# Performance work log

Measured on AMD Instinct MI355X. Metric: run time of the kernel, lower is better.

## Reference

```python
import jax, jax.numpy as jnp
import numpy as np

N_NODES = 50000
N_GRAPHS = 128
IN_DIM = 512
HID = 512
N_LAYERS = 3


def setup_inputs() -> dict:
    key = jax.random.key(0)
    ks = jax.random.split(key, 12)
    inp = {
        "x": jax.random.normal(ks[0], (N_NODES, IN_DIM), dtype=jnp.float32),
        "walk2": jax.random.randint(ks[1], (3, N_NODES), 0, N_NODES, dtype=jnp.int32),
        "walk3": jax.random.randint(ks[2], (4, N_NODES), 0, N_NODES, dtype=jnp.int32),
        "walk4": jax.random.randint(ks[3], (5, N_NODES), 0, N_NODES, dtype=jnp.int32),
        "batch": jnp.sort(jax.random.randint(ks[4], (N_NODES,), 0, N_GRAPHS, dtype=jnp.int32)),
    }
    dims = [IN_DIM, HID, HID]
    for i in range(N_LAYERS):
        scale = 1.0 / np.sqrt(dims[i])
        inp[f"W{i}"] = jax.random.normal(ks[5 + i], (dims[i], HID), dtype=jnp.float32) * scale
        inp[f"b{i}"] = jnp.zeros((HID,), dtype=jnp.float32)
    return inp


def _gather_sum(z, walk):
    # walk: [L, N] node indices -> sum of gathered embeddings, [N, H]
    L, N = walk.shape
    return jnp.take(z, walk.reshape(-1), axis=0).reshape(L, N, z.shape[1]).sum(0)


def reference(x, walk2, walk3, walk4, batch, W0, b0, W1, b1, W2, b2):
    layers = [(W0, b0), (W1, b1), (W2, b2)]
    path_batch = jnp.take(batch, walk2[0])  # [N]
    counts = jax.ops.segment_sum(jnp.ones((path_batch.shape[0],), jnp.float32),
                                 path_batch, num_segments=N_GRAPHS)
    denom = jnp.maximum(counts, 1.0)[:, None]  # avoid div-by-zero for empty graphs
    z = x
    g = []
    for W, b in layers:
        z = z @ W + b  # [N, H]
        path_emb = _gather_sum(z, walk2) + _gather_sum(z, walk3) + _gather_sum(z, walk4)
        pooled = jax.ops.segment_sum(path_emb, path_batch, num_segments=N_GRAPHS) / denom
        g.append(pooled)
    return jnp.concatenate(g, axis=1)  # [N_GRAPHS, 3*H]
```

## Files before the change

kernel.cpp:

```cpp
#include <hip/hip_runtime.h>

#define N_NODES 50000
#define N_GRAPHS 128
#define HID 512

#define KSPAN  208
#define KSPLIT 241
#define KPAD   (KSPAN * KSPLIT)

#define C8_OFF     0
#define C8_BYTES   ((size_t)N_GRAPHS * KPAD)
#define PSUM_OFF   (C8_OFF + C8_BYTES)
#define PSUM_BYTES ((size_t)N_GRAPHS * HID * 4)
#define COUNTS_OFF (PSUM_OFF + PSUM_BYTES)
#define ZERO_BYTES (COUNTS_OFF + 512)
#define CBF_OFF    ZERO_BYTES
#define CBF_BYTES  (2 * C8_BYTES)
#define PART_OFF   (CBF_OFF + CBF_BYTES)
#define PART_BYTES ((size_t)KSPLIT * N_GRAPHS * HID * 4)

typedef __attribute__((ext_vector_type(8))) short bf16x8;
typedef __attribute__((ext_vector_type(16))) float f32x16;

__global__ __launch_bounds__(256)
void build_c_kernel(const int* __restrict__ w2, const int* __restrict__ w3,
                    const int* __restrict__ w4, const int* __restrict__ batch,
                    unsigned int* __restrict__ C32, int* __restrict__ counts) {
    __shared__ int hist[N_GRAPHS];
    const int t = threadIdx.x;
    if (t < N_GRAPHS) hist[t] = 0;
    __syncthreads();
    const int i = blockIdx.x * 256 + t;
    if (i < N_NODES) {
        const int a = w2[i];
        const int g = batch[a];
        atomicAdd(&hist[g], 1);
        unsigned int* row = C32 + (size_t)g * (KPAD / 4);
        int nn[12];
        nn[0]  = a;
        nn[1]  = w2[N_NODES + i];
        nn[2]  = w2[2 * N_NODES + i];
        nn[3]  = w3[i];
        nn[4]  = w3[N_NODES + i];
        nn[5]  = w3[2 * N_NODES + i];
        nn[6]  = w3[3 * N_NODES + i];
        nn[7]  = w4[i];
        nn[8]  = w4[N_NODES + i];
        nn[9]  = w4[2 * N_NODES + i];
        nn[10] = w4[3 * N_NODES + i];
        nn[11] = w4[4 * N_NODES + i];
#pragma unroll
        for (int j = 0; j < 12; ++j) {
            const int nd = nn[j];
            atomicAdd(&row[nd >> 2], 1u << ((nd & 3) * 8));
        }
    }
    __syncthreads();
    if (t < N_GRAPHS) { const int hv = hist[t]; if (hv) atomicAdd(&counts[t], hv); }
}

__global__ __launch_bounds__(256)
void c8_to_bf16_kernel(const unsigned int* __restrict__ C32,
                       unsigned int* __restrict__ Cbf) {
    const int i = blockIdx.x * 256 + threadIdx.x;
    const int total = N_GRAPHS * (KPAD / 4);
    if (i >= total) return;
    const unsigned v = C32[i];
    const float f0 = (float)(v & 0xFFu);
    const float f1 = (float)((v >> 8) & 0xFFu);
    const float f2 = (float)((v >> 16) & 0xFFu);
    const float f3 = (float)(v >> 24);
    Cbf[2 * i]     = (__builtin_bit_cast(unsigned, f0) >> 16) |
                     (__builtin_bit_cast(unsigned, f1) & 0xFFFF0000u);
    Cbf[2 * i + 1] = (__builtin_bit_cast(unsigned, f2) >> 16) |
                     (__builtin_bit_cast(unsigned, f3) & 0xFFFF0000u);
}

template <int GUARD>
__device__ inline void make_b(const float* __restrict__ x, int k0, int h,
                              int col, bf16x8& bh, bf16x8& bl) {
    float v[8];
#pragma unroll
    for (int j = 0; j < 8; ++j) {
        const int k = k0 + 8 * h + j;
        v[j] = (!GUARD || k < N_NODES) ? x[(size_t)k * HID + col] : 0.f;
    }
    unsigned hw[4], lw[4];
#pragma unroll
    for (int j = 0; j < 4; ++j) {
        const unsigned u0 = __builtin_bit_cast(unsigned, v[2 * j]);
        const unsigned u1 = __builtin_bit_cast(unsigned, v[2 * j + 1]);
        const unsigned h0 = u0 & 0xFFFF0000u, h1 = u1 & 0xFFFF0000u;
        hw[j] = (h0 >> 16) | h1;
        const float r0 = v[2 * j] - __builtin_bit_cast(float, h0);
        const float r1 = v[2 * j + 1] - __builtin_bit_cast(float, h1);
        lw[j] = (__builtin_bit_cast(unsigned, r0) >> 16) |
                (__builtin_bit_cast(unsigned, r1) & 0xFFFF0000u);
    }
    uint4 uh = make_uint4(hw[0], hw[1], hw[2], hw[3]);
    uint4 ul = make_uint4(lw[0], lw[1], lw[2], lw[3]);
    bh = __builtin_bit_cast(bf16x8, uh);
    bl = __builtin_bit_cast(bf16x8, ul);
}

template <int ATOMIC>
__global__ __launch_bounds__(256, 2)
void pool_gemm2_kernel(const float* __restrict__ x,
                       const unsigned int* __restrict__ Cbf,
                       float* __restrict__ dst) {
    const int t = threadIdx.x;
    const int lane = t & 63;
    const int w = t >> 6;
    const int n = lane & 31;
    const int h = lane >> 5;
    const int colbase = (blockIdx.x * 4 + w) * 64;
    const int ks = blockIdx.y;
    const int kbase = ks * KSPAN;

    f32x16 acc[4][2];
#pragma unroll
    for (int mt = 0; mt < 4; ++mt)
#pragma unroll
        for (int nt = 0; nt < 2; ++nt)
#pragma unroll
            for (int r = 0; r < 16; ++r) acc[mt][nt][r] = 0.f;

    const int col0 = colbase + n;

    for (int s = 0; s < KSPAN / 16; ++s) {
        const int k0 = kbase + s * 16;

        bf16x8 af[4];
#pragma unroll
        for (int mt = 0; mt < 4; ++mt) {
            const unsigned int* ap =
                Cbf + (size_t)(mt * 32 + n) * (KPAD / 2) + (unsigned)(k0 + 8 * h) / 2;
            af[mt] = __builtin_bit_cast(bf16x8, *(const uint4*)ap);
        }

        bf16x8 bh0, bl0, bh1, bl1;
        if (k0 + 16 <= N_NODES) {
            make_b<0>(x, k0, h, col0, bh0, bl0);
            make_b<0>(x, k0, h, col0 + 32, bh1, bl1);
        } else {
            make_b<1>(x, k0, h, col0, bh0, bl0);
            make_b<1>(x, k0, h, col0 + 32, bh1, bl1);
        }

#pragma unroll
        for (int mt = 0; mt < 4; ++mt) {
            acc[mt][0] = __builtin_amdgcn_mfma_f32_32x32x16_bf16(af[mt], bh0, acc[mt][0], 0, 0, 0);
            acc[mt][0] = __builtin_amdgcn_mfma_f32_32x32x16_bf16(af[mt], bl0, acc[mt][0], 0, 0, 0);
            acc[mt][1] = __builtin_amdgcn_mfma_f32_32x32x16_bf16(af[mt], bh1, acc[mt][1], 0, 0, 0);
            acc[mt][1] = __builtin_amdgcn_mfma_f32_32x32x16_bf16(af[mt], bl1, acc[mt][1], 0, 0, 0);
        }
    }

    float* outp = ATOMIC ? dst : dst + (size_t)ks * (N_GRAPHS * HID);
#pragma unroll
    for (int mt = 0; mt < 4; ++mt)
#pragma unroll
        for (int nt = 0; nt < 2; ++nt) {
            const int col = colbase + nt * 32 + n;
#pragma unroll
            for (int r = 0; r < 16; ++r) {
                const int row = mt * 32 + (r & 3) + 8 * (r >> 2) + 4 * h;
                if (ATOMIC) atomicAdd(&outp[(size_t)row * HID + col], acc[mt][nt][r]);
                else        outp[(size_t)row * HID + col] = acc[mt][nt][r];
            }
        }
}

__global__ __launch_bounds__(256)
void reduce_part_kernel(const float* __restrict__ part, float* __restrict__ Psum) {
    const int id = blockIdx.x * 256 + threadIdx.x;
    float s0 = 0.f, s1 = 0.f, s2 = 0.f, s3 = 0.f;
    int k = 0;
    for (; k + 4 <= KSPLIT; k += 4) {
        s0 += part[(size_t)k * (N_GRAPHS * HID) + id];
        s1 += part[(size_t)(k + 1) * (N_GRAPHS * HID) + id];
        s2 += part[(size_t)(k + 2) * (N_GRAPHS * HID) + id];
        s3 += part[(size_t)(k + 3) * (N_GRAPHS * HID) + id];
    }
    for (; k < KSPLIT; ++k) s0 += part[(size_t)k * (N_GRAPHS * HID) + id];
    Psum[id] = (s0 + s1) + (s2 + s3);
}

__global__ __launch_bounds__(256)
void layer_gemm_kernel(const float* __restrict__ A, int lda, int scaleA,
                       const float* __restrict__ W,
                       const float* __restrict__ bias,
                       const int* __restrict__ counts,
                       float* __restrict__ out) {
    __shared__ float Alds[16][128];
    const int ct = blockIdx.x, rt = blockIdx.y, ksb = blockIdx.z;
    const int t = threadIdx.x;
    const int cc = ct * 64 + (t & 63);
    const int wv = t >> 6;
    const int k0 = ksb * 128;

    for (int idx = t; idx < 16 * 32; idx += 256) {
        const int rr = idx >> 5;
        const int kk = (idx & 31) * 4;
        const int row = rt * 16 + rr;
        float4 v = *(const float4*)&A[(size_t)row * lda + k0 + kk];
        if (scaleA) {
            const float inv = 1.f / (float)max(counts[row], 1);
            v.x *= inv; v.y *= inv; v.z *= inv; v.w *= inv;
        }
        *(float4*)&Alds[rr][kk] = v;
    }
    __syncthreads();

    const int r0 = rt * 16 + wv * 4;
    float a0 = 0.f, a1 = 0.f, a2 = 0.f, a3 = 0.f;
#pragma unroll 8
    for (int k = 0; k < 128; ++k) {
        const float wval = W[(size_t)(k0 + k) * HID + cc];
        a0 += Alds[wv * 4 + 0][k] * wval;
        a1 += Alds[wv * 4 + 1][k] * wval;
        a2 += Alds[wv * 4 + 2][k] * wval;
        a3 += Alds[wv * 4 + 3][k] * wval;
    }
    if (ksb == 0) {
        const float bc = bias[cc];
        a0 += (counts[r0 + 0] > 0 ? 12.f : 0.f) * bc;
        a1 += (counts[r0 + 1] > 0 ? 12.f : 0.f) * bc;
        a2 += (counts[r0 + 2] > 0 ? 12.f : 0.f) * bc;
        a3 += (counts[r0 + 3] > 0 ? 12.f : 0.f) * bc;
    }
    atomicAdd(&out[(size_t)(r0 + 0) * 1536 + cc], a0);
    atomicAdd(&out[(size_t)(r0 + 1) * 1536 + cc], a1);
    atomicAdd(&out[(size_t)(r0 + 2) * 1536 + cc], a2);
    atomicAdd(&out[(size_t)(r0 + 3) * 1536 + cc], a3);
}

extern "C" void kernel_launch(void* const* d_in, const int* in_sizes, int n_in,
                              void* d_out, int out_size, void* d_ws, size_t ws_size,
                              hipStream_t stream) {
    const float* x     = (const float*)d_in[0];
    const int*   w2    = (const int*)d_in[1];
    const int*   w3    = (const int*)d_in[2];
    const int*   w4    = (const int*)d_in[3];
    const int*   batch = (const int*)d_in[4];
    const float* W0    = (const float*)d_in[5];
    const float* b0    = (const float*)d_in[6];
    const float* W1    = (const float*)d_in[7];
    const float* b1    = (const float*)d_in[8];
    const float* W2    = (const float*)d_in[9];
    const float* b2    = (const float*)d_in[10];
    float* out = (float*)d_out;

    unsigned char* ws = (unsigned char*)d_ws;
    unsigned int* C32 = (unsigned int*)(ws + C8_OFF);
    float* Psum       = (float*)(ws + PSUM_OFF);
    int* counts       = (int*)(ws + COUNTS_OFF);
    unsigned int* Cbf = (unsigned int*)(ws + CBF_OFF);
    float* part       = (float*)(ws + PART_OFF);
    const bool use_part = ws_size >= PART_OFF + PART_BYTES;

    hipMemsetAsync(d_ws, 0, ZERO_BYTES, stream);
    hipMemsetAsync(d_out, 0, (size_t)out_size * 4, stream);

    build_c_kernel<<<(N_NODES + 255) / 256, 256, 0, stream>>>(w2, w3, w4, batch, C32, counts);

    const int cvt_total = N_GRAPHS * (KPAD / 4);
    c8_to_bf16_kernel<<<(cvt_total + 255) / 256, 256, 0, stream>>>(C32, Cbf);

    if (use_part) {
        pool_gemm2_kernel<0><<<dim3(2, KSPLIT), 256, 0, stream>>>(x, Cbf, part);
        reduce_part_kernel<<<256, 256, 0, stream>>>(part, Psum);
    } else {
        pool_gemm2_kernel<1><<<dim3(2, KSPLIT), 256, 0, stream>>>(x, Cbf, Psum);
    }

    layer_gemm_kernel<<<dim3(8, 8, 4), 256, 0, stream>>>(Psum, HID, 1, W0, b0, counts, out);
    layer_gemm_kernel<<<dim3(8, 8, 4), 256, 0, stream>>>(out, 1536, 0, W1, b1, counts, out + 512);
    layer_gemm_kernel<<<dim3(8, 8, 4), 256, 0, stream>>>(out + 512, 1536, 0, W2, b2, counts, out + 1024);
}
```

Before: 289.7 us.

## Restructure pooled GEMM with prepacked A fragments, LDS-staged x, fewer K splits

The count matrix is now converted once into a fragment-ordered packed layout, so each wave reads its A operand with one coalesced 16-byte load per lane. Tiles of x are staged into LDS with global_load_lds and shared by four waves per block, each covering a 32x32 output tile over two row blocks. The K span is doubled, which halves the number of partial sums written and then reduced. The hi/lo bf16 split of x is dropped and only the truncated high half is used, which halves the MFMA work but lowers the precision of the pooled sums.

```diff
diff --git a/kernel.cpp b/kernel.cpp
--- a/kernel.cpp
+++ b/kernel.cpp
@@ -4,9 +4,10 @@
 #define N_GRAPHS 128
 #define HID 512
 
-#define KSPAN  208
-#define KSPLIT 241
+#define KSPAN  416
+#define KSPLIT 121
 #define KPAD   (KSPAN * KSPLIT)
+#define NPANEL (KPAD / 16)
 
 #define C8_OFF     0
 #define C8_BYTES   ((size_t)N_GRAPHS * KPAD)
@@ -14,13 +15,15 @@
 #define PSUM_BYTES ((size_t)N_GRAPHS * HID * 4)
 #define COUNTS_OFF (PSUM_OFF + PSUM_BYTES)
 #define ZERO_BYTES (COUNTS_OFF + 512)
-#define CBF_OFF    ZERO_BYTES
-#define CBF_BYTES  (2 * C8_BYTES)
-#define PART_OFF   (CBF_OFF + CBF_BYTES)
+#define APACK_OFF  ZERO_BYTES
+#define APACK_BYTES ((size_t)NPANEL * 4 * 64 * 16)
+#define PART_OFF   (APACK_OFF + APACK_BYTES)
 #define PART_BYTES ((size_t)KSPLIT * N_GRAPHS * HID * 4)
 
 typedef __attribute__((ext_vector_type(8))) short bf16x8;
 typedef __attribute__((ext_vector_type(16))) float f32x16;
+typedef const __attribute__((address_space(1))) void* gas_t;
+typedef __attribute__((address_space(3))) void* las_t;
 
 __global__ __launch_bounds__(256)
 void build_c_kernel(const int* __restrict__ w2, const int* __restrict__ w3,
@@ -59,116 +62,108 @@
     if (t < N_GRAPHS) { const int hv = hist[t]; if (hv) atomicAdd(&counts[t], hv); }
 }
 
-__global__ __launch_bounds__(256)
-void c8_to_bf16_kernel(const unsigned int* __restrict__ C32,
-                       unsigned int* __restrict__ Cbf) {
-    const int i = blockIdx.x * 256 + threadIdx.x;
-    const int total = N_GRAPHS * (KPAD / 4);
-    if (i >= total) return;
-    const unsigned v = C32[i];
-    const float f0 = (float)(v & 0xFFu);
-    const float f1 = (float)((v >> 8) & 0xFFu);
-    const float f2 = (float)((v >> 16) & 0xFFu);
-    const float f3 = (float)(v >> 24);
-    Cbf[2 * i]     = (__builtin_bit_cast(unsigned, f0) >> 16) |
-                     (__builtin_bit_cast(unsigned, f1) & 0xFFFF0000u);
-    Cbf[2 * i + 1] = (__builtin_bit_cast(unsigned, f2) >> 16) |
-                     (__builtin_bit_cast(unsigned, f3) & 0xFFFF0000u);
-}
-
-template <int GUARD>
-__device__ inline void make_b(const float* __restrict__ x, int k0, int h,
-                              int col, bf16x8& bh, bf16x8& bl) {
-    float v[8];
-#pragma unroll
-    for (int j = 0; j < 8; ++j) {
-        const int k = k0 + 8 * h + j;
-        v[j] = (!GUARD || k < N_NODES) ? x[(size_t)k * HID + col] : 0.f;
-    }
-    unsigned hw[4], lw[4];
-#pragma unroll
-    for (int j = 0; j < 4; ++j) {
-        const unsigned u0 = __builtin_bit_cast(unsigned, v[2 * j]);
-        const unsigned u1 = __builtin_bit_cast(unsigned, v[2 * j + 1]);
-        const unsigned h0 = u0 & 0xFFFF0000u, h1 = u1 & 0xFFFF0000u;
-        hw[j] = (h0 >> 16) | h1;
-        const float r0 = v[2 * j] - __builtin_bit_cast(float, h0);
-        const float r1 = v[2 * j + 1] - __builtin_bit_cast(float, h1);
-        lw[j] = (__builtin_bit_cast(unsigned, r0) >> 16) |
-                (__builtin_bit_cast(unsigned, r1) & 0xFFFF0000u);
-    }
-    uint4 uh = make_uint4(hw[0], hw[1], hw[2], hw[3]);
-    uint4 ul = make_uint4(lw[0], lw[1], lw[2], lw[3]);
-    bh = __builtin_bit_cast(bf16x8, uh);
-    bl = __builtin_bit_cast(bf16x8, ul);
+__device__ inline unsigned pack_bf16(unsigned a, unsigned b) {
+    return (__builtin_bit_cast(unsigned, (float)a) >> 16) |
+           (__builtin_bit_cast(unsigned, (float)b) & 0xFFFF0000u);
+}
+
+__global__ __launch_bounds__(256)
+void c8_to_apack_kernel(const unsigned char* __restrict__ C8,
+                        uint4* __restrict__ Apack) {
+    const int kp = blockIdx.x;
+    const int t = threadIdx.x;
+    const int mt = t >> 6;
+    const int l = t & 63;
+    const int row = mt * 32 + (l & 31);
+    const int k0 = kp * 16 + 8 * (l >> 5);
+    const uint2 b = *(const uint2*)(C8 + (size_t)row * KPAD + k0);
+    uint4 o;
+    o.x = pack_bf16(b.x & 0xFFu, (b.x >> 8) & 0xFFu);
+    o.y = pack_bf16((b.x >> 16) & 0xFFu, b.x >> 24);
+    o.z = pack_bf16(b.y & 0xFFu, (b.y >> 8) & 0xFFu);
+    o.w = pack_bf16((b.y >> 16) & 0xFFu, b.y >> 24);
+    Apack[(size_t)(kp * 4 + mt) * 64 + l] = o;
 }
 
 template <int ATOMIC>
-__global__ __launch_bounds__(256, 2)
-void pool_gemm2_kernel(const float* __restrict__ x,
-                       const unsigned int* __restrict__ Cbf,
+__global__ __launch_bounds__(256, 4)
+void pool_gemm3_kernel(const float* __restrict__ x,
+                       const uint4* __restrict__ Apack,
                        float* __restrict__ dst) {
+    __shared__ float lbuf[32 * 64];
     const int t = threadIdx.x;
     const int lane = t & 63;
     const int w = t >> 6;
     const int n = lane & 31;
     const int h = lane >> 5;
-    const int colbase = (blockIdx.x * 4 + w) * 64;
+    const int nt = w & 1;
+    const int p = w >> 1;
+    const int colbase = blockIdx.x * 64;
     const int ks = blockIdx.y;
     const int kbase = ks * KSPAN;
 
-    f32x16 acc[4][2];
-#pragma unroll
-    for (int mt = 0; mt < 4; ++mt)
-#pragma unroll
-        for (int nt = 0; nt < 2; ++nt)
-#pragma unroll
-            for (int r = 0; r < 16; ++r) acc[mt][nt][r] = 0.f;
-
-    const int col0 = colbase + n;
-
-    for (int s = 0; s < KSPAN / 16; ++s) {
-        const int k0 = kbase + s * 16;
-
-        bf16x8 af[4];
-#pragma unroll
-        for (int mt = 0; mt < 4; ++mt) {
-            const unsigned int* ap =
-                Cbf + (size_t)(mt * 32 + n) * (KPAD / 2) + (unsigned)(k0 + 8 * h) / 2;
-            af[mt] = __builtin_bit_cast(bf16x8, *(const uint4*)ap);
-        }
-
-        bf16x8 bh0, bl0, bh1, bl1;
-        if (k0 + 16 <= N_NODES) {
-            make_b<0>(x, k0, h, col0, bh0, bl0);
-            make_b<0>(x, k0, h, col0 + 32, bh1, bl1);
+    f32x16 acc0, acc1;
+#pragma unroll
+    for (int r = 0; r < 16; ++r) { acc0[r] = 0.f; acc1[r] = 0.f; }
+
+    for (int ch = 0; ch < KSPAN / 32; ++ch) {
+        const int k0 = kbase + ch * 32;
+        if (k0 >= N_NODES) break;
+        if (k0 + 32 <= N_NODES) {
+#pragma unroll
+            for (int i = 0; i < 2; ++i) {
+                const int r = w * 8 + i * 4 + (lane >> 4);
+                const float* gp = x + (size_t)(k0 + r) * HID + colbase + (lane & 15) * 4;
+                las_t lp = (las_t)&lbuf[(w * 8 + i * 4) * 64];
+                __builtin_amdgcn_global_load_lds((gas_t)gp, lp, 16, 0, 0);
+            }
         } else {
-            make_b<1>(x, k0, h, col0, bh0, bl0);
-            make_b<1>(x, k0, h, col0 + 32, bh1, bl1);
-        }
-
-#pragma unroll
-        for (int mt = 0; mt < 4; ++mt) {
-            acc[mt][0] = __builtin_amdgcn_mfma_f32_32x32x16_bf16(af[mt], bh0, acc[mt][0], 0, 0, 0);
-            acc[mt][0] = __builtin_amdgcn_mfma_f32_32x32x16_bf16(af[mt], bl0, acc[mt][0], 0, 0, 0);
-            acc[mt][1] = __builtin_amdgcn_mfma_f32_32x32x16_bf16(af[mt], bh1, acc[mt][1], 0, 0, 0);
-            acc[mt][1] = __builtin_amdgcn_mfma_f32_32x32x16_bf16(af[mt], bl1, acc[mt][1], 0, 0, 0);
-        }
+#pragma unroll
+            for (int j = 0; j < 8; ++j) {
+                const int idx = t + j * 256;
+                const int r = idx >> 6, c = idx & 63;
+                const int kg = k0 + r;
+                lbuf[idx] = (kg < N_NODES) ? x[(size_t)kg * HID + colbase + c] : 0.f;
+            }
+        }
+        __syncthreads();
+
+        const int kp0 = k0 >> 4;
+#pragma unroll
+        for (int kk = 0; kk < 2; ++kk) {
+            unsigned bw[4];
+#pragma unroll
+            for (int j2 = 0; j2 < 4; ++j2) {
+                const int kl = kk * 16 + 8 * h + 2 * j2;
+                const unsigned u0 = __builtin_bit_cast(unsigned, lbuf[kl * 64 + nt * 32 + n]);
+                const unsigned u1 = __builtin_bit_cast(unsigned, lbuf[(kl + 1) * 64 + nt * 32 + n]);
+                bw[j2] = (u0 >> 16) | (u1 & 0xFFFF0000u);
+            }
+            const uint4 bu = make_uint4(bw[0], bw[1], bw[2], bw[3]);
+            const bf16x8 bf = __builtin_bit_cast(bf16x8, bu);
+            const bf16x8 a0 = __builtin_bit_cast(bf16x8,
+                Apack[(size_t)((kp0 + kk) * 4 + 2 * p) * 64 + lane]);
+            const bf16x8 a1 = __builtin_bit_cast(bf16x8,
+                Apack[(size_t)((kp0 + kk) * 4 + 2 * p + 1) * 64 + lane]);
+            acc0 = __builtin_amdgcn_mfma_f32_32x32x16_bf16(a0, bf, acc0, 0, 0, 0);
+            acc1 = __builtin_amdgcn_mfma_f32_32x32x16_bf16(a1, bf, acc1, 0, 0, 0);
+        }
+        __syncthreads();
     }
 
     float* outp = ATOMIC ? dst : dst + (size_t)ks * (N_GRAPHS * HID);
-#pragma unroll
-    for (int mt = 0; mt < 4; ++mt)
-#pragma unroll
-        for (int nt = 0; nt < 2; ++nt) {
-            const int col = colbase + nt * 32 + n;
-#pragma unroll
-            for (int r = 0; r < 16; ++r) {
-                const int row = mt * 32 + (r & 3) + 8 * (r >> 2) + 4 * h;
-                if (ATOMIC) atomicAdd(&outp[(size_t)row * HID + col], acc[mt][nt][r]);
-                else        outp[(size_t)row * HID + col] = acc[mt][nt][r];
-            }
-        }
+    const int col = colbase + nt * 32 + n;
+#pragma unroll
+    for (int r = 0; r < 16; ++r) {
+        const int row0 = 2 * p * 32 + (r & 3) + 8 * (r >> 2) + 4 * h;
+        if (ATOMIC) {
+            atomicAdd(&outp[(size_t)row0 * HID + col], acc0[r]);
+            atomicAdd(&outp[(size_t)(row0 + 32) * HID + col], acc1[r]);
+        } else {
+            outp[(size_t)row0 * HID + col] = acc0[r];
+            outp[(size_t)(row0 + 32) * HID + col] = acc1[r];
+        }
+    }
 }
 
 __global__ __launch_bounds__(256)
@@ -251,27 +246,25 @@
     const float* b2    = (const float*)d_in[10];
     float* out = (float*)d_out;
 
-    unsigned char* ws = (unsigned char*)d_ws;
-    unsigned int* C32 = (unsigned int*)(ws + C8_OFF);
-    float* Psum       = (float*)(ws + PSUM_OFF);
-    int* counts       = (int*)(ws + COUNTS_OFF);
-    unsigned int* Cbf = (unsigned int*)(ws + CBF_OFF);
-    float* part       = (float*)(ws + PART_OFF);
+    unsigned char* ws  = (unsigned char*)d_ws;
+    unsigned int* C32  = (unsigned int*)(ws + C8_OFF);
+    float* Psum        = (float*)(ws + PSUM_OFF);
+    int* counts        = (int*)(ws + COUNTS_OFF);
+    uint4* Apack       = (uint4*)(ws + APACK_OFF);
+    float* part        = (float*)(ws + PART_OFF);
     const bool use_part = ws_size >= PART_OFF + PART_BYTES;
 
     hipMemsetAsync(d_ws, 0, ZERO_BYTES, stream);
     hipMemsetAsync(d_out, 0, (size_t)out_size * 4, stream);
 
     build_c_kernel<<<(N_NODES + 255) / 256, 256, 0, stream>>>(w2, w3, w4, batch, C32, counts);
-
-    const int cvt_total = N_GRAPHS * (KPAD / 4);
-    c8_to_bf16_kernel<<<(cvt_total + 255) / 256, 256, 0, stream>>>(C32, Cbf);
+    c8_to_apack_kernel<<<NPANEL, 256, 0, stream>>>((const unsigned char*)C32, Apack);
 
     if (use_part) {
-        pool_gemm2_kernel<0><<<dim3(2, KSPLIT), 256, 0, stream>>>(x, Cbf, part);
+        pool_gemm3_kernel<0><<<dim3(8, KSPLIT), 256, 0, stream>>>(x, Apack, part);
         reduce_part_kernel<<<256, 256, 0, stream>>>(part, Psum);
     } else {
-        pool_gemm2_kernel<1><<<dim3(2, KSPLIT), 256, 0, stream>>>(x, Cbf, Psum);
+        pool_gemm3_kernel<1><<<dim3(8, KSPLIT), 256, 0, stream>>>(x, Apack, Psum);
     }
 
     layer_gemm_kernel<<<dim3(8, 8, 4), 256, 0, stream>>>(Psum, HID, 1, W0, b0, counts, out);
```

Measured after the change: 279.6 us. 3.5% less time.
